# Kernel tuning notes

Hardware: AMD Instinct MI355X
Metric: run time of the kernel (lower is better)

## Reference

```python
import jax, jax.numpy as jnp
import numpy as np

VOCAB, NUM_CLASSES, E, H = 50257, 20, 64, 64
B, T = 128, 2048


def setup_inputs() -> dict:
    key = jax.random.key(0)
    ks = jax.random.split(key, 16)
    s_ih = 1.0 / np.sqrt(H)
    u = lambda k, shape: jax.random.uniform(k, shape, jnp.float32, -s_ih, s_ih)
    return {
        'tokens': jax.random.randint(ks[0], (B, T), 0, VOCAB),
        'emb': jax.random.normal(ks[1], (VOCAB, E), jnp.float32),
        # forward-direction GRU params (PyTorch layout: [3H, *], gate order r,z,n)
        'wih_f': u(ks[2], (3 * H, E)), 'whh_f': u(ks[3], (3 * H, H)),
        'bih_f': u(ks[4], (3 * H,)), 'bhh_f': u(ks[5], (3 * H,)),
        # backward-direction GRU params
        'wih_b': u(ks[6], (3 * H, E)), 'whh_b': u(ks[7], (3 * H, H)),
        'bih_b': u(ks[8], (3 * H,)), 'bhh_b': u(ks[9], (3 * H,)),
        # classifier: Linear(4H -> H), GELU, Linear(H -> C)
        'w1': u(ks[10], (H, 4 * H)), 'b1': u(ks[11], (H,)),
        'w2': u(ks[12], (NUM_CLASSES, H)), 'b2': u(ks[13], (NUM_CLASSES,)),
    }


def _gru_dir(x, wih, whh, bih, bhh):
    # x: [B, T, E] -> outputs [B, T, H]; PyTorch GRU gate math, gates (r, z, n)
    xg = jnp.einsum('bte,ge->tbg', x, wih) + bih  # precompute input projections [T,B,3H]
    h0 = jnp.zeros((x.shape[0], H), x.dtype)

    def step(h, xg_t):
        hg = h @ whh.T + bhh
        xr, xz, xn = jnp.split(xg_t, 3, axis=-1)
        hr, hz, hn = jnp.split(hg, 3, axis=-1)
        r = jax.nn.sigmoid(xr + hr)
        z = jax.nn.sigmoid(xz + hz)
        n = jnp.tanh(xn + r * hn)
        h_new = (1.0 - z) * n + z * h
        return h_new, h_new

    _, hs = jax.lax.scan(step, h0, xg)  # hs: [T, B, H]
    return hs.transpose(1, 0, 2)


def reference(tokens, emb, wih_f, whh_f, bih_f, bhh_f,
              wih_b, whh_b, bih_b, bhh_b, w1, b1, w2, b2):
    x = emb[tokens]  # [B, T, E]
    h_fwd = _gru_dir(x, wih_f, whh_f, bih_f, bhh_f)
    h_bwd = _gru_dir(x[:, ::-1], wih_b, whh_b, bih_b, bhh_b)[:, ::-1]
    encoded = jnp.concatenate([h_fwd, h_bwd], axis=-1)  # [B, T, 2H]
    feats = jnp.concatenate([encoded.mean(axis=1), encoded.max(axis=1)], axis=-1)  # [B, 4H]
    hid = jax.nn.gelu(feats @ w1.T + b1, approximate=False)
    return hid @ w2.T + b2  # [B, C]
```

## Files before the change

kernel.cpp:

```cpp
#include <hip/hip_runtime.h>
#include <hip/hip_bf16.h>
#include <math.h>

#define VOCAB 50257
#define NCLS 20
#define EDIM 64
#define HDIM 64
#define BATCH 128
#define TLEN 2048

typedef float v2f __attribute__((ext_vector_type(2)));

__device__ float g_P[(size_t)2 * VOCAB * 192];
__device__ float g_feats[BATCH * 256];

__device__ __forceinline__ float fast_rcp(float x) { return __builtin_amdgcn_rcpf(x); }

__device__ __forceinline__ float fsigmoid(float x) {
    return fast_rcp(1.f + __expf(-x));
}
__device__ __forceinline__ float ftanh(float x) {
    float e = __expf(2.f * x);
    return 1.f - 2.f * fast_rcp(e + 1.f);
}

__global__ __launch_bounds__(384) void precompute_P(
    const float* __restrict__ emb,
    const float* __restrict__ wih_f, const float* __restrict__ bih_f,
    const float* __restrict__ wih_b, const float* __restrict__ bih_b)
{
    const int t = threadIdx.x;
    const int dir = t / 192;
    const int g = t % 192;
    const float* wih = dir ? wih_b : wih_f;
    const float* bih = dir ? bih_b : bih_f;

    float w[64];
#pragma unroll
    for (int e = 0; e < 64; e += 4) {
        float4 v = *(const float4*)(wih + (size_t)g * 64 + e);
        w[e] = v.x; w[e + 1] = v.y; w[e + 2] = v.z; w[e + 3] = v.w;
    }
    const float bias = bih[g];
    float* Pd = g_P + (size_t)dir * VOCAB * 192;

    for (int v = blockIdx.x; v < VOCAB; v += gridDim.x) {
        const float4* er = (const float4*)(emb + (size_t)v * 64);
        float acc = bias;
#pragma unroll
        for (int e4 = 0; e4 < 16; e4++) {
            float4 x = er[e4];
            acc = fmaf(x.x, w[4 * e4 + 0], acc);
            acc = fmaf(x.y, w[4 * e4 + 1], acc);
            acc = fmaf(x.z, w[4 * e4 + 2], acc);
            acc = fmaf(x.w, w[4 * e4 + 3], acc);
        }
        Pd[(size_t)v * 192 + g] = acc;
    }
}

__global__ __launch_bounds__(64, 1) void gru_seq(
    const int* __restrict__ tokens,
    const float* __restrict__ whh_f, const float* __restrict__ bhh_f,
    const float* __restrict__ whh_b, const float* __restrict__ bhh_b)
{
    const int lane = threadIdx.x;
    const int blk = blockIdx.x;
    const int b = blk >> 1;
    const int dir = blk & 1;
    const float* whh = dir ? whh_b : whh_f;
    const float* bhh = dir ? bhh_b : bhh_f;
    const float* Pd = g_P + (size_t)dir * VOCAB * 192;

    __shared__ __align__(16) float h_lds[64];
    __shared__ int tok_lds[TLEN];

    for (int t = lane; t < TLEN; t += 64) tok_lds[t] = tokens[b * TLEN + t];

    v2f wr[32], wz[32], wn[32];
    {
        const float* pr = whh + (size_t)(0 + lane) * 64;
        const float* pz = whh + (size_t)(64 + lane) * 64;
        const float* pn = whh + (size_t)(128 + lane) * 64;
#pragma unroll
        for (int k = 0; k < 16; k++) {
            float4 a = *(const float4*)(pr + 4 * k);
            wr[2 * k] = (v2f){a.x, a.y}; wr[2 * k + 1] = (v2f){a.z, a.w};
            float4 c = *(const float4*)(pz + 4 * k);
            wz[2 * k] = (v2f){c.x, c.y}; wz[2 * k + 1] = (v2f){c.z, c.w};
            float4 d = *(const float4*)(pn + 4 * k);
            wn[2 * k] = (v2f){d.x, d.y}; wn[2 * k + 1] = (v2f){d.z, d.w};
        }
    }
    const float br = bhh[lane], bz = bhh[64 + lane], bn = bhh[128 + lane];

    h_lds[lane] = 0.f;
    float h = 0.f, sum = 0.f, mx = -INFINITY;
    __syncthreads();

    auto tok_at = [&](int s) -> int {
        int ss = s < TLEN ? s : TLEN - 1;
        return tok_lds[dir ? (TLEN - 1 - ss) : ss];
    };

    float xrA, xzA, xnA, xrB, xzB, xnB, xrC, xzC, xnC;
    {
        const float* r0 = Pd + (size_t)tok_at(0) * 192;
        xrA = r0[lane]; xzA = r0[64 + lane]; xnA = r0[128 + lane];
        const float* r1 = Pd + (size_t)tok_at(1) * 192;
        xrB = r1[lane]; xzB = r1[64 + lane]; xnB = r1[128 + lane];
        const float* r2 = Pd + (size_t)tok_at(2) * 192;
        xrC = r2[lane]; xzC = r2[64 + lane]; xnC = r2[128 + lane];
    }

    for (int s = 0; s < TLEN; s++) {
        const float* rp = Pd + (size_t)tok_at(s + 3) * 192;
        float pxr = rp[lane], pxz = rp[64 + lane], pxn = rp[128 + lane];

        v2f ar0 = {0.f, 0.f}, ar1 = {0.f, 0.f};
        v2f az0 = {0.f, 0.f}, az1 = {0.f, 0.f};
        v2f an0 = {0.f, 0.f}, an1 = {0.f, 0.f};
#pragma unroll
        for (int k = 0; k < 16; k++) {
            float4 h4 = *(const float4*)(h_lds + 4 * k);
            v2f h01 = {h4.x, h4.y}, h23 = {h4.z, h4.w};
            ar0 = __builtin_elementwise_fma(h01, wr[2 * k], ar0);
            az0 = __builtin_elementwise_fma(h01, wz[2 * k], az0);
            an0 = __builtin_elementwise_fma(h01, wn[2 * k], an0);
            ar1 = __builtin_elementwise_fma(h23, wr[2 * k + 1], ar1);
            az1 = __builtin_elementwise_fma(h23, wz[2 * k + 1], az1);
            an1 = __builtin_elementwise_fma(h23, wn[2 * k + 1], an1);
        }
        float hr = (ar0.x + ar0.y) + (ar1.x + ar1.y);
        float hz = (az0.x + az0.y) + (az1.x + az1.y);
        float hn = (an0.x + an0.y) + (an1.x + an1.y);

        float r = fsigmoid(xrA + hr + br);
        float z = fsigmoid(xzA + hz + bz);
        float n = ftanh(xnA + r * (hn + bn));
        h = fmaf(z, h - n, n);
        sum += h;
        mx = fmaxf(mx, h);

        __syncthreads();
        h_lds[lane] = h;
        __syncthreads();

        xrA = xrB; xzA = xzB; xnA = xnB;
        xrB = xrC; xzB = xzC; xnB = xnC;
        xrC = pxr; xzC = pxz; xnC = pxn;
    }

    g_feats[b * 256 + dir * 64 + lane] = sum * (1.f / TLEN);
    g_feats[b * 256 + 128 + dir * 64 + lane] = mx;
}

__global__ __launch_bounds__(64) void classifier(
    const float* __restrict__ w1, const float* __restrict__ b1,
    const float* __restrict__ w2, const float* __restrict__ b2,
    float* __restrict__ out)
{
    const int b = blockIdx.x;
    const int i = threadIdx.x;
    __shared__ float f[256];
    __shared__ float hid[64];
    for (int c = i; c < 256; c += 64) f[c] = g_feats[b * 256 + c];
    __syncthreads();

    float acc = b1[i];
    const float* wrow = w1 + (size_t)i * 256;
#pragma unroll 16
    for (int c = 0; c < 256; c++) acc = fmaf(f[c], wrow[c], acc);
    hid[i] = acc * 0.5f * (1.f + erff(acc * 0.70710678118654752f));
    __syncthreads();

    if (i < NCLS) {
        float o = b2[i];
        const float* w2r = w2 + (size_t)i * 64;
#pragma unroll
        for (int j = 0; j < 64; j++) o = fmaf(hid[j], w2r[j], o);
        out[b * NCLS + i] = o;
    }
}

extern "C" void kernel_launch(void* const* d_in, const int* in_sizes, int n_in,
                              void* d_out, int out_size, void* d_ws, size_t ws_size,
                              hipStream_t stream) {
    const int*   tokens = (const int*)  d_in[0];
    const float* emb    = (const float*)d_in[1];
    const float* wih_f  = (const float*)d_in[2];
    const float* whh_f  = (const float*)d_in[3];
    const float* bih_f  = (const float*)d_in[4];
    const float* bhh_f  = (const float*)d_in[5];
    const float* wih_b  = (const float*)d_in[6];
    const float* whh_b  = (const float*)d_in[7];
    const float* bih_b  = (const float*)d_in[8];
    const float* bhh_b  = (const float*)d_in[9];
    const float* w1     = (const float*)d_in[10];
    const float* b1     = (const float*)d_in[11];
    const float* w2     = (const float*)d_in[12];
    const float* b2     = (const float*)d_in[13];
    float* out = (float*)d_out;

    precompute_P<<<1024, 384, 0, stream>>>(emb, wih_f, bih_f, wih_b, bih_b);
    gru_seq<<<2 * BATCH, 64, 0, stream>>>(tokens, whh_f, bhh_f, whh_b, bhh_b);
    classifier<<<BATCH, 64, 0, stream>>>(w1, b1, w2, b2, out);
}
```

Before: 1.083 ms.

## Drop barriers in single-wave GRU loop, deepen prefetch, pair vocab rows

Result: faster. 977.9 us (-9.7%).

```diff
diff --git a/kernel.cpp b/kernel.cpp
--- a/kernel.cpp
+++ b/kernel.cpp
@@ -44,18 +44,26 @@
     const float bias = bih[g];
     float* Pd = g_P + (size_t)dir * VOCAB * 192;
 
-    for (int v = blockIdx.x; v < VOCAB; v += gridDim.x) {
-        const float4* er = (const float4*)(emb + (size_t)v * 64);
-        float acc = bias;
+    for (int v = blockIdx.x * 2; v < VOCAB; v += gridDim.x * 2) {
+        const int v1ok = (v + 1 < VOCAB);
+        const float4* e0 = (const float4*)(emb + (size_t)v * 64);
+        const float4* e1 = (const float4*)(emb + (size_t)(v1ok ? v + 1 : v) * 64);
+        float a0 = bias, a1 = bias;
 #pragma unroll
         for (int e4 = 0; e4 < 16; e4++) {
-            float4 x = er[e4];
-            acc = fmaf(x.x, w[4 * e4 + 0], acc);
-            acc = fmaf(x.y, w[4 * e4 + 1], acc);
-            acc = fmaf(x.z, w[4 * e4 + 2], acc);
-            acc = fmaf(x.w, w[4 * e4 + 3], acc);
+            float4 x = e0[e4];
+            float4 y = e1[e4];
+            a0 = fmaf(x.x, w[4 * e4 + 0], a0);
+            a1 = fmaf(y.x, w[4 * e4 + 0], a1);
+            a0 = fmaf(x.y, w[4 * e4 + 1], a0);
+            a1 = fmaf(y.y, w[4 * e4 + 1], a1);
+            a0 = fmaf(x.z, w[4 * e4 + 2], a0);
+            a1 = fmaf(y.z, w[4 * e4 + 2], a1);
+            a0 = fmaf(x.w, w[4 * e4 + 3], a0);
+            a1 = fmaf(y.w, w[4 * e4 + 3], a1);
         }
-        Pd[(size_t)v * 192 + g] = acc;
+        Pd[(size_t)v * 192 + g] = a0;
+        if (v1ok) Pd[(size_t)(v + 1) * 192 + g] = a1;
     }
 }
 
@@ -73,9 +81,13 @@
     const float* Pd = g_P + (size_t)dir * VOCAB * 192;
 
     __shared__ __align__(16) float h_lds[64];
-    __shared__ int tok_lds[TLEN];
-
-    for (int t = lane; t < TLEN; t += 64) tok_lds[t] = tokens[b * TLEN + t];
+    __shared__ __align__(16) int tok_lds[TLEN];
+
+    {
+        const int4* src = (const int4*)(tokens + (size_t)b * TLEN);
+        int4* dst = (int4*)tok_lds;
+        for (int t = lane; t < TLEN / 4; t += 64) dst[t] = src[t];
+    }
 
     v2f wr[32], wz[32], wn[32];
     {
@@ -96,26 +108,27 @@
 
     h_lds[lane] = 0.f;
     float h = 0.f, sum = 0.f, mx = -INFINITY;
-    __syncthreads();
 
     auto tok_at = [&](int s) -> int {
         int ss = s < TLEN ? s : TLEN - 1;
         return tok_lds[dir ? (TLEN - 1 - ss) : ss];
     };
 
-    float xrA, xzA, xnA, xrB, xzB, xnB, xrC, xzC, xnC;
-    {
-        const float* r0 = Pd + (size_t)tok_at(0) * 192;
-        xrA = r0[lane]; xzA = r0[64 + lane]; xnA = r0[128 + lane];
-        const float* r1 = Pd + (size_t)tok_at(1) * 192;
-        xrB = r1[lane]; xzB = r1[64 + lane]; xnB = r1[128 + lane];
-        const float* r2 = Pd + (size_t)tok_at(2) * 192;
-        xrC = r2[lane]; xzC = r2[64 + lane]; xnC = r2[128 + lane];
-    }
-
+    float xr[4], xz[4], xn[4];
+#pragma unroll
+    for (int d = 0; d < 4; d++) {
+        const float* rd = Pd + (size_t)tok_at(d) * 192;
+        xr[d] = rd[lane]; xz[d] = rd[64 + lane]; xn[d] = rd[128 + lane];
+    }
+    int tokN = tok_at(4);
+
+#pragma unroll 4
     for (int s = 0; s < TLEN; s++) {
-        const float* rp = Pd + (size_t)tok_at(s + 3) * 192;
+        const int slot = s & 3;
+
+        const float* rp = Pd + (size_t)tokN * 192;
         float pxr = rp[lane], pxz = rp[64 + lane], pxn = rp[128 + lane];
+        tokN = tok_at(s + 5);
 
         v2f ar0 = {0.f, 0.f}, ar1 = {0.f, 0.f};
         v2f az0 = {0.f, 0.f}, az1 = {0.f, 0.f};
@@ -135,20 +148,16 @@
         float hz = (az0.x + az0.y) + (az1.x + az1.y);
         float hn = (an0.x + an0.y) + (an1.x + an1.y);
 
-        float r = fsigmoid(xrA + hr + br);
-        float z = fsigmoid(xzA + hz + bz);
-        float n = ftanh(xnA + r * (hn + bn));
+        float r = fsigmoid(xr[slot] + hr + br);
+        float z = fsigmoid(xz[slot] + hz + bz);
+        float n = ftanh(xn[slot] + r * (hn + bn));
         h = fmaf(z, h - n, n);
         sum += h;
         mx = fmaxf(mx, h);
 
-        __syncthreads();
         h_lds[lane] = h;
-        __syncthreads();
-
-        xrA = xrB; xzA = xzB; xnA = xnB;
-        xrB = xrC; xzB = xzC; xnB = xnC;
-        xrC = pxr; xzC = pxz; xnC = pxn;
+
+        xr[slot] = pxr; xz[slot] = pxz; xn[slot] = pxn;
     }
 
     g_feats[b * 256 + dir * 64 + lane] = sum * (1.f / TLEN);
```
